# Kernel optimization log

Hardware: AMD Instinct MI355X
Metric: run time of the kernel (lower is better)

## Reference

```python
import jax, jax.numpy as jnp
import numpy as np

B, SEQ_LEN, ENC_IN, C_OUT = 128, 512, 21, 21
PRED_LEN, D_MODEL, N_HEADS, D_FF = 96, 512, 8, 2048
E_LAYERS = 2
PATCH_LEN, STRIDE = 16, 8
NUM_PATCH = (SEQ_LEN - PATCH_LEN) // STRIDE + 1  # 63
MODES = min(32, NUM_PATCH // 2)  # 31 (mode_select='low' -> index = range(MODES))
K_MA = 25
EPS = 1e-5
DH = D_MODEL // N_HEADS  # 64


def setup_inputs() -> dict:
    key = jax.random.key(0)
    ks = jax.random.split(key, 16)
    s = 0.02
    fscale = 1.0 / (D_MODEL * D_MODEL)
    return {
        'x_enc': jax.random.normal(ks[0], (B, SEQ_LEN, ENC_IN), jnp.float32),
        'x_mark_enc': jax.random.normal(ks[1], (B, SEQ_LEN, 4), jnp.float32),
        'x_dec': jax.random.normal(ks[2], (B, 144, ENC_IN), jnp.float32),
        'x_mark_dec': jax.random.normal(ks[3], (B, 144, 4), jnp.float32),
        'patch_W': s * jax.random.normal(ks[4], (D_MODEL, PATCH_LEN * ENC_IN), jnp.float32),
        'patch_b': jnp.zeros((D_MODEL,), jnp.float32),
        'Wq': s * jax.random.normal(ks[5], (E_LAYERS, D_MODEL, D_MODEL), jnp.float32),
        'bq': jnp.zeros((E_LAYERS, D_MODEL), jnp.float32),
        'Wo': s * jax.random.normal(ks[6], (E_LAYERS, D_MODEL, D_MODEL), jnp.float32),
        'bo': jnp.zeros((E_LAYERS, D_MODEL), jnp.float32),
        'four_wr': fscale * jax.random.uniform(ks[7], (E_LAYERS, N_HEADS, DH, DH, MODES), jnp.float32),
        'four_wi': fscale * jax.random.uniform(ks[8], (E_LAYERS, N_HEADS, DH, DH, MODES), jnp.float32),
        'conv1_W': s * jax.random.normal(ks[9], (E_LAYERS, D_FF, D_MODEL), jnp.float32),
        'conv2_W': s * jax.random.normal(ks[10], (E_LAYERS, D_MODEL, D_FF), jnp.float32),
        'norm_gamma': jnp.ones((D_MODEL,), jnp.float32),
        'norm_beta': jnp.zeros((D_MODEL,), jnp.float32),
        'head_W': s * jax.random.normal(ks[11], (PRED_LEN * C_OUT, NUM_PATCH * D_MODEL), jnp.float32),
        'head_b': jnp.zeros((PRED_LEN * C_OUT,), jnp.float32),
        'trend_W': s * jax.random.normal(ks[12], (PRED_LEN, SEQ_LEN), jnp.float32),
        'trend_b': jnp.zeros((PRED_LEN,), jnp.float32),
    }


def series_decomp(x, k=K_MA):
    # x: [B, L, C]; replicate-pad ends by (k-1)//2, moving mean via cumsum
    pad = (k - 1) // 2
    front = jnp.repeat(x[:, :1, :], pad, axis=1)
    end = jnp.repeat(x[:, -1:, :], pad, axis=1)
    xp = jnp.concatenate([front, x, end], axis=1)
    c = jnp.cumsum(xp, axis=1)
    c = jnp.concatenate([jnp.zeros_like(c[:, :1]), c], axis=1)
    mean = (c[:, k:] - c[:, :-k]) / k
    return x - mean, mean


def my_layernorm(x, g, b):
    mu = x.mean(-1, keepdims=True)
    var = ((x - mu) ** 2).mean(-1, keepdims=True)
    xh = (x - mu) / jnp.sqrt(var + EPS) * g + b
    return xh - xh.mean(axis=1, keepdims=True)


def fourier_block(q, wr, wi):
    # q: [B, L, H, E] -> torch FourierBlock (low-freq modes 0..MODES-1)
    Bq, L, H, E = q.shape
    xs = q.transpose(0, 2, 3, 1)                       # [B,H,E,L]
    x_ft = jnp.fft.rfft(xs, axis=-1)                   # [B,H,E,L//2+1]
    W = wr + 1j * wi                                   # [H,E,F,M] complex
    out_sel = jnp.einsum('bhem,hefm->bhfm', x_ft[..., :MODES], W)
    out_ft = jnp.zeros(x_ft.shape, x_ft.dtype).at[..., :MODES].set(out_sel)
    y = jnp.fft.irfft(out_ft, n=L, axis=-1)            # [B,H,E,L]
    # torch does out.view(B, L, -1) on contiguous [B,H,E,L]; flat reshape is identical
    return y.reshape(Bq, L, H * E)


def encoder_layer(x, Wq_l, bq_l, Wo_l, bo_l, wr, wi, c1, c2):
    Bq, L, D = x.shape
    q = (x @ Wq_l.T + bq_l).reshape(Bq, L, N_HEADS, DH)
    new_x = fourier_block(q, wr, wi) @ Wo_l.T + bo_l
    x, _ = series_decomp(x + new_x)
    y = jax.nn.gelu(x @ c1.T, approximate=False) @ c2.T  # conv1d k=1 == matmul, no bias
    res, _ = series_decomp(x + y)
    return res


def _forward(x_enc, patch_W, patch_b, Wq, bq, Wo, bo, four_wr, four_wi,
             conv1_W, conv2_W, norm_gamma, norm_beta, head_W, head_b, trend_W, trend_b):
    seasonal, trend = series_decomp(x_enc)
    # trend_projection over time axis: [B,L,C] -> [B,P,C]
    trend_out = jnp.einsum('blc,pl->bpc', trend, trend_W) + trend_b[None, :, None]
    # patching (unfold over time per channel, then mix channels)
    xs = seasonal.transpose(0, 2, 1)                   # [B,N,L]
    idx = STRIDE * jnp.arange(NUM_PATCH)[:, None] + jnp.arange(PATCH_LEN)[None, :]
    xp = xs[:, :, idx]                                 # [B,N,P,plen]
    xp = xp.transpose(0, 2, 1, 3).reshape(B, NUM_PATCH, ENC_IN * PATCH_LEN)
    enc = xp @ patch_W.T + patch_b                     # [B,P,D]
    for l in range(E_LAYERS):
        enc = encoder_layer(enc, Wq[l], bq[l], Wo[l], bo[l],
                            four_wr[l], four_wi[l], conv1_W[l], conv2_W[l])
    enc = my_layernorm(enc, norm_gamma, norm_beta)
    seasonal_out = (enc.reshape(B, -1) @ head_W.T + head_b).reshape(B, PRED_LEN, C_OUT)
    return seasonal_out + trend_out


def reference(x_enc, x_mark_enc, x_dec, x_mark_dec, patch_W, patch_b, Wq, bq, Wo, bo,
              four_wr, four_wi, conv1_W, conv2_W, norm_gamma, norm_beta,
              head_W, head_b, trend_W, trend_b):
    # x_mark_enc / x_dec / x_mark_dec are accepted but unused, as in the torch forward
    return _forward(x_enc, patch_W, patch_b, Wq, bq, Wo, bo, four_wr, four_wi,
                    conv1_W, conv2_W, norm_gamma, norm_beta, head_W, head_b, trend_W, trend_b)
```

## Files before the change

### kernel.cpp

```cpp
#include <hip/hip_runtime.h>
#include <math.h>

#define B_ 128
#define T_ 512
#define C_ 21
#define L_ 63
#define D_ 512
#define H_ 8
#define DH_ 64
#define MODES_ 31
#define FF_ 2048
#define P_ 96
#define KMA 25
#define PAD 12
#define NOUT (P_*C_)
#define KHEAD (L_*D_)
#define ML (B_*L_)

typedef __attribute__((ext_vector_type(8))) short short8;
typedef __attribute__((ext_vector_type(4))) float f32x4;

__device__ __forceinline__ unsigned short f2b(float f) {
    union { float f; unsigned u; } v; v.f = f;
    unsigned r = v.u + 0x7FFFu + ((v.u >> 16) & 1u);
    return (unsigned short)(r >> 16);
}
__device__ __forceinline__ float b2f(unsigned short u) {
    union { unsigned u; float f; } v; v.u = ((unsigned)u) << 16;
    return v.f;
}
__device__ __forceinline__ void gld_lds16(const void* g, void* l) {
    __builtin_amdgcn_global_load_lds(
        (const __attribute__((address_space(1))) unsigned int*)g,
        (__attribute__((address_space(3))) unsigned int*)l, 16, 0, 0);
}

__global__ void prep_k(const float* __restrict__ Wq, const float* __restrict__ Wo,
                       const float* __restrict__ c1, const float* __restrict__ c2,
                       unsigned short* __restrict__ WqB, unsigned short* __restrict__ WoB,
                       unsigned short* __restrict__ c1B, unsigned short* __restrict__ c2B,
                       const float* __restrict__ pW, unsigned short* __restrict__ pWB,
                       float* __restrict__ cosT, float* __restrict__ sinT) {
    int i = blockIdx.x * 256 + threadIdx.x;
    if (i < 262144) {
        const float* src = (i < 131072) ? Wq : Wo;
        unsigned short* dst = (i < 131072) ? WqB : WoB;
        int j = i & 131071;
        float4 v = ((const float4*)src)[j];
        uint2 p; p.x = (unsigned)f2b(v.x) | ((unsigned)f2b(v.y) << 16);
        p.y = (unsigned)f2b(v.z) | ((unsigned)f2b(v.w) << 16);
        ((uint2*)dst)[j] = p;
    } else if (i < 1310720) {
        int j = i - 262144;
        const float* src = (j < 524288) ? c1 : c2;
        unsigned short* dst = (j < 524288) ? c1B : c2B;
        j &= 524287;
        float4 v = ((const float4*)src)[j];
        uint2 p; p.x = (unsigned)f2b(v.x) | ((unsigned)f2b(v.y) << 16);
        p.y = (unsigned)f2b(v.z) | ((unsigned)f2b(v.w) << 16);
        ((uint2*)dst)[j] = p;
    } else if (i < 1359872) {
        int j = i - 1310720;
        int row = j / 96, c4 = j % 96;
        uint2 p; p.x = 0; p.y = 0;
        if (c4 < 84) {
            float4 v = *(const float4*)(pW + (size_t)row * 336 + c4 * 4);
            p.x = (unsigned)f2b(v.x) | ((unsigned)f2b(v.y) << 16);
            p.y = (unsigned)f2b(v.z) | ((unsigned)f2b(v.w) << 16);
        }
        ((uint2*)pWB)[j] = p;
    } else if (i < 1361888) {
        int j = i - 1359872;
        int m = j / 63, l = j % 63;
        if (m >= MODES_) { cosT[j] = 0.f; sinT[j] = 0.f; }
        else {
            int r = (m * l) % 63;
            double a = 6.283185307179586476925286766559 * (double)r / 63.0;
            cosT[j] = (float)cos(a); sinT[j] = (float)sin(a);
        }
    }
}

__global__ void decomp_input_k(const float* __restrict__ x,
                               unsigned short* __restrict__ seasB,
                               unsigned short* __restrict__ trendB) {
    int idx = blockIdx.x * 256 + threadIdx.x;
    if (idx >= B_ * C_ * 16) return;
    int tc = idx & 15; int rc = idx >> 4; int c = rc % C_; int b = rc / C_;
    const float* xb = x + (size_t)b * T_ * C_ + c;
    int t0 = tc * 32;
    float sum = 0.f;
    #pragma unroll
    for (int i = -PAD; i <= PAD; ++i) {
        int tt = t0 + i; tt = tt < 0 ? 0 : (tt > T_-1 ? T_-1 : tt);
        sum += xb[(size_t)tt * C_];
    }
    for (int t = t0; t < t0 + 32; ++t) {
        float mean = sum * (1.f / KMA);
        float xv = xb[(size_t)t * C_];
        size_t o = ((size_t)b * T_ + t) * C_ + c;
        seasB[o]  = f2b(xv - mean);
        trendB[o] = f2b(mean);
        int add = t + 13 > T_-1 ? T_-1 : t + 13;
        int rem = t - 12 < 0 ? 0 : t - 12;
        sum += xb[(size_t)add * C_] - xb[(size_t)rem * C_];
    }
}

__global__ void patches_k(const unsigned short* __restrict__ seasB,
                          unsigned short* __restrict__ xpB) {
    int idx = blockIdx.x * 256 + threadIdx.x;
    if (idx >= B_*L_*384) return;
    int col = idx % 384; int r = idx / 384; int n = r % L_; int b = r / L_;
    unsigned short v = 0;
    if (col < 336) {
        int c = col >> 4; int j = col & 15;
        v = seasB[((size_t)b * T_ + 8*n + j) * C_ + c];
    }
    xpB[idx] = v;
}

__global__ __launch_bounds__(256) void trend_mfma(
    const unsigned short* __restrict__ trendB, const float* __restrict__ tW,
    const float* __restrict__ tb, const float* __restrict__ hb,
    float* __restrict__ outT)
{
    __shared__ unsigned short Asl[64*32];
    __shared__ unsigned short Wsl[96*32];
    int bm = blockIdx.x;
    int t = threadIdx.x, wave = t >> 6, lane = t & 63;
    int wr = wave >> 1, wc = wave & 1, g2 = lane >> 4, rl = lane & 15;
    f32x4 acc[2][3] = {};
    int ar = t >> 2, aslot = t & 3;
    int rowg = bm*64 + ar; int ab = rowg / 21, ac = rowg % 21;
    for (int k0 = 0; k0 < 512; k0 += 32) {
        __syncthreads();
        {
            unsigned short vals[8];
            int kb = k0 + aslot*8;
            #pragma unroll
            for (int j = 0; j < 8; ++j)
                vals[j] = trendB[((size_t)ab * T_ + kb + j) * C_ + ac];
            int phys = aslot ^ ((ar>>1)&3);
            *(uint4*)&Asl[ar*32 + phys*8] = *(const uint4*)vals;
        }
        #pragma unroll
        for (int i = 0; i < 3; ++i) {
            int idx = t + 256*i;
            int r = idx >> 3, c4 = idx & 7;
            float4 w4 = *(const float4*)(tW + (size_t)r * T_ + k0 + c4*4);
            uint2 p; p.x = (unsigned)f2b(w4.x) | ((unsigned)f2b(w4.y) << 16);
            p.y = (unsigned)f2b(w4.z) | ((unsigned)f2b(w4.w) << 16);
            *(uint2*)&Wsl[r*32 + (((c4>>1) ^ ((r>>1)&3)) << 3) + ((c4&1) << 2)] = p;
        }
        __syncthreads();
        short8 af[2], wf[3];
        #pragma unroll
        for (int m = 0; m < 2; ++m) {
            int r = wr*32 + m*16 + rl;
            af[m] = *(const short8*)&Asl[r*32 + ((g2 ^ ((r>>1)&3)) << 3)];
        }
        #pragma unroll
        for (int n = 0; n < 3; ++n) {
            int r = wc*48 + n*16 + rl;
            wf[n] = *(const short8*)&Wsl[r*32 + ((g2 ^ ((r>>1)&3)) << 3)];
        }
        #pragma unroll
        for (int m = 0; m < 2; ++m)
            #pragma unroll
            for (int n = 0; n < 3; ++n)
                acc[m][n] = __builtin_amdgcn_mfma_f32_16x16x32_bf16(af[m], wf[n], acc[m][n], 0,0,0);
    }
    #pragma unroll
    for (int n = 0; n < 3; ++n) {
        int p = wc*48 + n*16 + rl;
        float bias = tb[p];
        #pragma unroll
        for (int m = 0; m < 2; ++m)
            #pragma unroll
            for (int j = 0; j < 4; ++j) {
                int rg = bm*64 + wr*32 + m*16 + g2*4 + j;
                int b = rg / 21, c = rg % 21;
                outT[(size_t)b * NOUT + p*21 + c] = acc[m][n][j] + bias + hb[p*21 + c];
            }
    }
}

__global__ __launch_bounds__(256) void gemm_mfma(
    const unsigned short* __restrict__ A,
    const unsigned short* __restrict__ W,
    const float* __restrict__ bias,
    float* __restrict__ Cf,
    unsigned short* __restrict__ Cb,
    int M, int N, int K, int act)
{
    __shared__ unsigned short Asl[2][64*64];
    __shared__ unsigned short Wsl[2][128*64];
    int bm = blockIdx.y, bn = blockIdx.x;
    int t = threadIdx.x;
    int wave = t >> 6, lane = t & 63;
    int wr = wave >> 1, wc = wave & 1;
    int g2 = lane >> 4, rl = lane & 15;
    int lr8 = lane >> 3, l7 = lane & 7;
    f32x4 acc[2][4] = {};
    const unsigned short* Ab = A + (size_t)(bm*64) * K;
    const unsigned short* Wb = W + (size_t)(bn*128) * K;

    #pragma unroll
    for (int i = 0; i < 2; ++i) {
        int seg = wave*2 + i;
        int r = seg*8 + lr8;
        int ko = (l7 ^ (r & 7)) << 3;
        gld_lds16(Ab + (size_t)r*K + ko, &Asl[0][seg*512]);
    }
    #pragma unroll
    for (int i = 0; i < 4; ++i) {
        int seg = wave*4 + i;
        int r = seg*8 + lr8;
        int ko = (l7 ^ (r & 7)) << 3;
        gld_lds16(Wb + (size_t)r*K + ko, &Wsl[0][seg*512]);
    }

    int cur = 0;
    for (int k0 = 0; k0 < K; k0 += 64, cur ^= 1) {
        __syncthreads();
        if (k0 + 64 < K) {
            int kn = k0 + 64;
            #pragma unroll
            for (int i = 0; i < 2; ++i) {
                int seg = wave*2 + i;
                int r = seg*8 + lr8;
                int ko = (l7 ^ (r & 7)) << 3;
                gld_lds16(Ab + (size_t)r*K + kn + ko, &Asl[cur^1][seg*512]);
            }
            #pragma unroll
            for (int i = 0; i < 4; ++i) {
                int seg = wave*4 + i;
                int r = seg*8 + lr8;
                int ko = (l7 ^ (r & 7)) << 3;
                gld_lds16(Wb + (size_t)r*K + kn + ko, &Wsl[cur^1][seg*512]);
            }
        }
        short8 af[2][2], wf[2][4];
        #pragma unroll
        for (int sub = 0; sub < 2; ++sub) {
            #pragma unroll
            for (int m = 0; m < 2; ++m) {
                int r = wr*32 + m*16 + rl;
                af[sub][m] = *(const short8*)&Asl[cur][r*64 + (((sub*4+g2) ^ (r&7)) << 3)];
            }
            #pragma unroll
            for (int n = 0; n < 4; ++n) {
                int r = wc*64 + n*16 + rl;
                wf[sub][n] = *(const short8*)&Wsl[cur][r*64 + (((sub*4+g2) ^ (r&7)) << 3)];
            }
        }
        #pragma unroll
        for (int sub = 0; sub < 2; ++sub)
            #pragma unroll
            for (int m = 0; m < 2; ++m)
                #pragma unroll
                for (int n = 0; n < 4; ++n)
                    acc[m][n] = __builtin_amdgcn_mfma_f32_16x16x32_bf16(af[sub][m], wf[sub][n], acc[m][n], 0,0,0);
    }

    int crow0 = bm*64 + wr*32;
    int ccol0 = bn*128 + wc*64;
    #pragma unroll
    for (int n = 0; n < 4; ++n) {
        int col = ccol0 + n*16 + rl;
        float bv = bias ? bias[col] : 0.f;
        #pragma unroll
        for (int m = 0; m < 2; ++m) {
            #pragma unroll
            for (int j = 0; j < 4; ++j) {
                int row = crow0 + m*16 + g2*4 + j;
                float x = acc[m][n][j] + bv;
                if (act == 1) x = 0.5f * x * (1.f + erff(x * 0.70710678118654752f));
                size_t ix = (size_t)row * N + col;
                if (Cf) Cf[ix] = x;
                if (Cb) Cb[ix] = f2b(x);
            }
        }
    }
}

__global__ __launch_bounds__(256) void fourier1_k(
    const float* __restrict__ q, const float* __restrict__ cosT, const float* __restrict__ sinT,
    float* __restrict__ Xre_g, float* __restrict__ Xim_g)
{
    __shared__ float qs[63][64];
    __shared__ float ct[2016], st[2016];
    int b = blockIdx.x >> 3, h = blockIdx.x & 7;
    int t = threadIdx.x;
    for (int idx = t; idx < 1008; idx += 256) {
        int l = idx >> 4, e4 = idx & 15;
        *(float4*)&qs[l][e4*4] = *(const float4*)(q + ((size_t)(b*63 + l))*512 + h*64 + e4*4);
    }
    for (int idx = t; idx < 504; idx += 256) {
        *(float4*)&ct[idx*4] = *(const float4*)(cosT + idx*4);
        *(float4*)&st[idx*4] = *(const float4*)(sinT + idx*4);
    }
    __syncthreads();
    int mm = t & 31, g = t >> 5;
    float re[8] = {}, im[8] = {};
    for (int l = 0; l < 63; ++l) {
        float c = ct[mm*63 + l], s = st[mm*63 + l];
        #pragma unroll
        for (int j = 0; j < 8; ++j) {
            float v = qs[l][g*8 + j];
            re[j] = fmaf(v, c, re[j]);
            im[j] = fmaf(-v, s, im[j]);
        }
    }
    if (mm < MODES_) {
        size_t base = ((size_t)(h*MODES_ + mm)*128 + b)*64 + g*8;
        *(float4*)&Xre_g[base]   = *(float4*)&re[0];
        *(float4*)&Xre_g[base+4] = *(float4*)&re[4];
        *(float4*)&Xim_g[base]   = *(float4*)&im[0];
        *(float4*)&Xim_g[base+4] = *(float4*)&im[4];
    }
}

__global__ __launch_bounds__(256) void fourier2_k(
    const float* __restrict__ Xre_g, const float* __restrict__ Xim_g,
    const float* __restrict__ wr, const float* __restrict__ wi,
    float* __restrict__ Ore_g, float* __restrict__ Oim_g)
{
    __shared__ unsigned short Xr[128*64], Xi[128*64];
    __shared__ unsigned short Wr[64*64], Wi[64*64], Wn[64*64];
    int h = blockIdx.x / MODES_, mm = blockIdx.x % MODES_;
    int t = threadIdx.x;
    size_t xbase = ((size_t)(h*MODES_ + mm)) * 128 * 64;
    #pragma unroll
    for (int i = 0; i < 8; ++i) {
        int idx = t + 256*i;
        int r = idx >> 4, c4 = idx & 15;
        int ad = r*64 + (((c4>>1) ^ (r&7)) << 3) + ((c4&1) << 2);
        float4 v = *(const float4*)(Xre_g + xbase + (size_t)r*64 + c4*4);
        uint2 p; p.x = (unsigned)f2b(v.x) | ((unsigned)f2b(v.y) << 16);
        p.y = (unsigned)f2b(v.z) | ((unsigned)f2b(v.w) << 16);
        *(uint2*)&Xr[ad] = p;
        v = *(const float4*)(Xim_g + xbase + (size_t)r*64 + c4*4);
        p.x = (unsigned)f2b(v.x) | ((unsigned)f2b(v.y) << 16);
        p.y = (unsigned)f2b(v.z) | ((unsigned)f2b(v.w) << 16);
        *(uint2*)&Xi[ad] = p;
    }
    #pragma unroll
    for (int i = 0; i < 2; ++i) {
        int idx = t + 256*i;
        int f = idx >> 3, oct = idx & 7;
        unsigned short wrv[8], wiv[8], wnv[8];
        #pragma unroll
        for (int j = 0; j < 8; ++j) {
            int e = oct*8 + j;
            size_t a = (((size_t)(h*64 + e))*64 + f)*MODES_ + mm;
            wrv[j] = f2b(wr[a]);
            wiv[j] = f2b(wi[a]);
            wnv[j] = wiv[j] ^ 0x8000u;
        }
        int ad = f*64 + ((oct ^ (f&7)) << 3);
        *(uint4*)&Wr[ad] = *(const uint4*)wrv;
        *(uint4*)&Wi[ad] = *(const uint4*)wiv;
        *(uint4*)&Wn[ad] = *(const uint4*)wnv;
    }
    __syncthreads();
    int wave = t >> 6, lane = t & 63;
    int wv = wave >> 1, wc = wave & 1;
    int g2 = lane >> 4, rl = lane & 15;
    f32x4 ar[4][2] = {}, ai[4][2] = {};
    #pragma unroll
    for (int sub = 0; sub < 2; ++sub) {
        short8 xr[4], xi[4], br[2], bi[2], bn[2];
        #pragma unroll
        for (int m = 0; m < 4; ++m) {
            int r = wv*64 + m*16 + rl;
            int off = r*64 + (((sub*4+g2) ^ (r&7)) << 3);
            xr[m] = *(const short8*)&Xr[off];
            xi[m] = *(const short8*)&Xi[off];
        }
        #pragma unroll
        for (int n = 0; n < 2; ++n) {
            int r = wc*32 + n*16 + rl;
            int off = r*64 + (((sub*4+g2) ^ (r&7)) << 3);
            br[n] = *(const short8*)&Wr[off];
            bi[n] = *(const short8*)&Wi[off];
            bn[n] = *(const short8*)&Wn[off];
        }
        #pragma unroll
        for (int m = 0; m < 4; ++m)
            #pragma unroll
            for (int n = 0; n < 2; ++n) {
                ar[m][n] = __builtin_amdgcn_mfma_f32_16x16x32_bf16(xr[m], br[n], ar[m][n], 0,0,0);
                ar[m][n] = __builtin_amdgcn_mfma_f32_16x16x32_bf16(xi[m], bn[n], ar[m][n], 0,0,0);
                ai[m][n] = __builtin_amdgcn_mfma_f32_16x16x32_bf16(xr[m], bi[n], ai[m][n], 0,0,0);
                ai[m][n] = __builtin_amdgcn_mfma_f32_16x16x32_bf16(xi[m], br[n], ai[m][n], 0,0,0);
            }
    }
    #pragma unroll
    for (int m = 0; m < 4; ++m)
        #pragma unroll
        for (int n = 0; n < 2; ++n)
            #pragma unroll
            for (int j = 0; j < 4; ++j) {
                int b = wv*64 + m*16 + g2*4 + j;
                int f = wc*32 + n*16 + rl;
                Ore_g[xbase + (size_t)b*64 + f] = ar[m][n][j];
                Oim_g[xbase + (size_t)b*64 + f] = ai[m][n][j];
            }
}

__global__ __launch_bounds__(256) void fourier3_k(
    const float* __restrict__ Ore_g, const float* __restrict__ Oim_g,
    const float* __restrict__ cosT, const float* __restrict__ sinT,
    unsigned short* __restrict__ yB)
{
    __shared__ float Ore[31][64], Oim[31][64];
    __shared__ float ct[2016], st[2016];
    int b = blockIdx.x >> 3, h = blockIdx.x & 7;
    int t = threadIdx.x;
    for (int idx = t; idx < 496; idx += 256) {
        int m = idx >> 4, e4 = idx & 15;
        size_t a = ((size_t)(h*MODES_ + m)*128 + b)*64 + e4*4;
        *(float4*)&Ore[m][e4*4] = *(const float4*)(Ore_g + a);
        *(float4*)&Oim[m][e4*4] = *(const float4*)(Oim_g + a);
    }
    for (int idx = t; idx < 504; idx += 256) {
        *(float4*)&ct[idx*4] = *(const float4*)(cosT + idx*4);
        *(float4*)&st[idx*4] = *(const float4*)(sinT + idx*4);
    }
    __syncthreads();
    int f = t & 63, w = t >> 6;
    int l0 = w*16;
    float y[16];
    float r0 = Ore[0][f];
    #pragma unroll
    for (int i = 0; i < 16; ++i) y[i] = r0;
    for (int m = 1; m < MODES_; ++m) {
        float re2 = 2.f*Ore[m][f], im2 = 2.f*Oim[m][f];
        #pragma unroll
        for (int i = 0; i < 16; ++i) {
            y[i] = fmaf(re2, ct[m*63 + l0 + i], y[i]);
            y[i] = fmaf(-im2, st[m*63 + l0 + i], y[i]);
        }
    }
    int nl = (w == 3) ? 15 : 16;
    unsigned short* yo = yB + ((size_t)(b*512) + h*64 + f) * 63 + l0;
    for (int i = 0; i < nl; ++i) yo[i] = f2b(y[i] * (1.f/63.f));
}

__global__ void decomp_add_k(const unsigned short* __restrict__ X,
                             const unsigned short* __restrict__ Yv,
                             unsigned short* __restrict__ outB) {
    int idx = blockIdx.x * 256 + threadIdx.x;
    if (idx >= B_*D_) return;
    int b = idx >> 9, d = idx & 511;
    const unsigned short* xp = X  + (size_t)b * L_ * D_ + d;
    const unsigned short* yp = Yv + (size_t)b * L_ * D_ + d;
    unsigned short* ob = outB + (size_t)b * L_ * D_ + d;
    #define RD(l) (b2f(xp[(size_t)(l) * D_]) + b2f(yp[(size_t)(l) * D_]))
    float sum = 13.f * RD(0);
    #pragma unroll
    for (int j = 1; j <= 12; ++j) sum += RD(j);
    for (int l = 0; l < L_; ++l) {
        float res = RD(l) - sum * (1.f / KMA);
        ob[(size_t)l * D_] = f2b(res);
        int add = l + 13 > L_-1 ? L_-1 : l + 13;
        int rem = l - 12 < 0 ? 0 : l - 12;
        sum += RD(add) - RD(rem);
    }
    #undef RD
}

__global__ __launch_bounds__(256) void ln_colmean_k(
    const unsigned short* __restrict__ Xb, const float* __restrict__ g,
    const float* __restrict__ bt, unsigned short* __restrict__ outB)
{
    __shared__ unsigned short lds[63][512];
    int b = blockIdx.x;
    int w = threadIdx.x >> 6, lane = threadIdx.x & 63;
    for (int i = 0; i < 16; ++i) {
        int row = w*16 + i;
        if (row >= 63) break;
        const unsigned short* x = Xb + ((size_t)(b*63 + row))*512 + lane*8;
        uint4 raw = *(const uint4*)x;
        const unsigned short* rp = (const unsigned short*)&raw;
        float v[8]; float s = 0.f, s2 = 0.f;
        #pragma unroll
        for (int j = 0; j < 8; ++j) { v[j] = b2f(rp[j]); s += v[j]; s2 += v[j]*v[j]; }
        #pragma unroll
        for (int o = 32; o > 0; o >>= 1) { s += __shfl_down(s, o); s2 += __shfl_down(s2, o); }
        s = __shfl(s, 0); s2 = __shfl(s2, 0);
        float mu = s * (1.f/D_);
        float var = s2 * (1.f/D_) - mu*mu;
        float rs = rsqrtf(var + 1e-5f);
        unsigned short o16[8];
        #pragma unroll
        for (int j = 0; j < 8; ++j) {
            int d = lane*8 + j;
            o16[j] = f2b((v[j] - mu) * rs * g[d] + bt[d]);
        }
        *(uint4*)&lds[row][lane*8] = *(const uint4*)o16;
    }
    __syncthreads();
    #pragma unroll
    for (int i = 0; i < 2; ++i) {
        int d = threadIdx.x + 256*i;
        float s = 0.f;
        for (int l = 0; l < 63; ++l) s += b2f(lds[l][d]);
        s *= (1.f / 63.f);
        for (int l = 0; l < 63; ++l)
            outB[((size_t)(b*63 + l))*512 + d] = f2b(b2f(lds[l][d]) - s);
    }
}

__global__ __launch_bounds__(256) void head_mfma(
    const unsigned short* __restrict__ A,
    const float* __restrict__ W,
    float* __restrict__ parts)
{
    __shared__ float red[128][48];
    int nt = blockIdx.x;
    int kc = blockIdx.y;
    int wv = threadIdx.x >> 6, lane = threadIdx.x & 63;
    int rl = lane & 15, g2 = lane >> 4;
    f32x4 acc[8][3] = {};
    const unsigned short* Ab = A + (size_t)rl * KHEAD;
    const float* Wb = W + (size_t)(nt*48 + rl) * KHEAD;
    int kbeg = kc*2688 + wv*672 + g2*8;

    for (int ks = 0; ks < 21; ++ks) {
        int k = kbeg + ks*32;
        short8 af[8];
        #pragma unroll
        for (int m = 0; m < 8; ++m)
            af[m] = *(const short8*)(Ab + (size_t)(m*16) * KHEAD + k);
        short8 wf[3];
        #pragma unroll
        for (int n = 0; n < 3; ++n) {
            float4 lo = *(const float4*)(Wb + (size_t)(n*16) * KHEAD + k);
            float4 hi = *(const float4*)(Wb + (size_t)(n*16) * KHEAD + k + 4);
            unsigned short u[8] = { f2b(lo.x), f2b(lo.y), f2b(lo.z), f2b(lo.w),
                                    f2b(hi.x), f2b(hi.y), f2b(hi.z), f2b(hi.w) };
            wf[n] = *(const short8*)u;
        }
        #pragma unroll
        for (int m = 0; m < 8; ++m)
            #pragma unroll
            for (int n = 0; n < 3; ++n)
                acc[m][n] = __builtin_amdgcn_mfma_f32_16x16x32_bf16(af[m], wf[n], acc[m][n], 0,0,0);
    }

    for (int w = 0; w < 4; ++w) {
        if (wv == w) {
            #pragma unroll
            for (int m = 0; m < 8; ++m)
                #pragma unroll
                for (int n = 0; n < 3; ++n)
                    #pragma unroll
                    for (int j = 0; j < 4; ++j) {
                        int row = m*16 + g2*4 + j, col = n*16 + rl;
                        if (w == 0) red[row][col] = acc[m][n][j];
                        else        red[row][col] += acc[m][n][j];
                    }
        }
        __syncthreads();
    }
    float* pout = parts + (size_t)kc * (B_*NOUT);
    for (int idx = threadIdx.x; idx < 128*48; idx += 256) {
        int row = idx / 48, col = idx % 48;
        pout[(size_t)row * NOUT + nt*48 + col] = red[row][col];
    }
}

__global__ void reduce_k(const float* __restrict__ trendout, const float* __restrict__ parts,
                         float* __restrict__ out) {
    int i = blockIdx.x * 256 + threadIdx.x;
    if (i >= 64512) return;
    float4 s = ((const float4*)trendout)[i];
    for (int kc = 0; kc < 12; ++kc) {
        float4 p = ((const float4*)parts)[(size_t)kc * 64512 + i];
        s.x += p.x; s.y += p.y; s.z += p.z; s.w += p.w;
    }
    ((float4*)out)[i] = s;
}

extern "C" void kernel_launch(void* const* d_in, const int* in_sizes, int n_in,
                              void* d_out, int out_size, void* d_ws, size_t ws_size,
                              hipStream_t stream) {
    const float* x_enc   = (const float*)d_in[0];
    const float* patch_W = (const float*)d_in[4];
    const float* patch_b = (const float*)d_in[5];
    const float* Wq      = (const float*)d_in[6];
    const float* bq      = (const float*)d_in[7];
    const float* Wo      = (const float*)d_in[8];
    const float* bo      = (const float*)d_in[9];
    const float* four_wr = (const float*)d_in[10];
    const float* four_wi = (const float*)d_in[11];
    const float* c1      = (const float*)d_in[12];
    const float* c2      = (const float*)d_in[13];
    const float* gamma   = (const float*)d_in[14];
    const float* beta    = (const float*)d_in[15];
    const float* head_W  = (const float*)d_in[16];
    const float* head_b  = (const float*)d_in[17];
    const float* trend_W = (const float*)d_in[18];
    const float* trend_b = (const float*)d_in[19];
    float* out = (float*)d_out;
    float* ws  = (float*)d_ws;

    unsigned short* seasB  = (unsigned short*)ws;
    unsigned short* trendB = (unsigned short*)(ws + 688128);
    unsigned short* xpB    = (unsigned short*)(ws + 1376256);
    unsigned short* bufAb  = (unsigned short*)(ws + 2924544);
    unsigned short* tmpB16 = (unsigned short*)(ws + 4988928);
    unsigned short* tmp2   = (unsigned short*)(ws + 7053312);
    unsigned short* bufCb  = (unsigned short*)(ws + 9117696);
    float* qF    = ws + 11182080;
    float* Ore_g = qF;
    float* Oim_g = qF + 2031616;
    float* big   = ws + 15310848;
    unsigned short* hidB = (unsigned short*)big;
    float* Xre_g = big;
    float* Xim_g = big + 2031616;
    unsigned short* WqB = (unsigned short*)(ws + 23568384);
    unsigned short* WoB = (unsigned short*)(ws + 23830528);
    unsigned short* c1B = (unsigned short*)(ws + 24092672);
    unsigned short* c2B = (unsigned short*)(ws + 25141248);
    unsigned short* pWB = (unsigned short*)(ws + 26189824);
    float* cosT = ws + 26288128;
    float* sinT = ws + 26290144;
    float* trendout = ws + 26292160;
    float* parts = ws + 26550208;

    auto cdiv = [](int a, int b) { return (a + b - 1) / b; };

    prep_k<<<5321,256,0,stream>>>(Wq, Wo, c1, c2, WqB, WoB, c1B, c2B, patch_W, pWB, cosT, sinT);
    decomp_input_k<<<cdiv(B_*C_*16,256),256,0,stream>>>(x_enc, seasB, trendB);
    patches_k<<<cdiv(B_*L_*384,256),256,0,stream>>>(seasB, xpB);
    trend_mfma<<<42,256,0,stream>>>(trendB, trend_W, trend_b, head_b, trendout);

    gemm_mfma<<<dim3(4,126),256,0,stream>>>(xpB, pWB, patch_b, (float*)nullptr, bufAb, ML, 512, 384, 0);

    for (int l = 0; l < 2; ++l) {
        const unsigned short* WqB_l = WqB + (size_t)l*512*512;
        const unsigned short* WoB_l = WoB + (size_t)l*512*512;
        const unsigned short* c1B_l = c1B + (size_t)l*FF_*D_;
        const unsigned short* c2B_l = c2B + (size_t)l*D_*FF_;
        const float* bq_l = bq + (size_t)l*512;
        const float* bo_l = bo + (size_t)l*512;
        const float* wr_l = four_wr + (size_t)l*H_*DH_*DH_*MODES_;
        const float* wi_l = four_wi + (size_t)l*H_*DH_*DH_*MODES_;

        gemm_mfma<<<dim3(4,126),256,0,stream>>>(bufAb, WqB_l, bq_l, qF, (unsigned short*)nullptr, ML, 512, 512, 0);
        fourier1_k<<<B_*H_,256,0,stream>>>(qF, cosT, sinT, Xre_g, Xim_g);
        fourier2_k<<<H_*MODES_,256,0,stream>>>(Xre_g, Xim_g, wr_l, wi_l, Ore_g, Oim_g);
        fourier3_k<<<B_*H_,256,0,stream>>>(Ore_g, Oim_g, cosT, sinT, tmpB16);
        gemm_mfma<<<dim3(4,126),256,0,stream>>>(tmpB16, WoB_l, bo_l, (float*)nullptr, tmp2, ML, 512, 512, 0);
        decomp_add_k<<<cdiv(B_*D_,256),256,0,stream>>>(bufAb, tmp2, bufCb);
        gemm_mfma<<<dim3(16,126),256,0,stream>>>(bufCb, c1B_l, (const float*)nullptr, (float*)nullptr, hidB, ML, FF_, 512, 1);
        gemm_mfma<<<dim3(4,126),256,0,stream>>>(hidB, c2B_l, (const float*)nullptr, (float*)nullptr, tmp2, ML, 512, FF_, 0);
        decomp_add_k<<<cdiv(B_*D_,256),256,0,stream>>>(bufCb, tmp2, bufAb);
    }

    ln_colmean_k<<<B_,256,0,stream>>>(bufAb, gamma, beta, tmpB16);
    head_mfma<<<dim3(42,12),256,0,stream>>>(tmpB16, head_W, parts);
    reduce_k<<<cdiv(64512,256),256,0,stream>>>(trendout, parts, out);
}
```

Measured before the change: 556.1 us.

## Split-K Wo/conv2 GEMMs and trend GEMM, fuse decomp with patch extraction

Adds a split-K dimension to the generic GEMM, used with two K-chunks for the Wo and conv2 projections. The two bf16 partial outputs are summed inside decomp_add_k, which now also holds the 63-row column in registers instead of re-reading it. The trend GEMM is split four ways and writes into the head partials buffer, so one reduce covers both. Input decomposition and patch extraction are fused into one per-batch kernel through LDS. The aim is more blocks in flight for the GEMMs that had only 504 blocks, and fewer launches and round trips through memory. The cost is extra partial-sum traffic and bf16 rounding of partial sums before they are added.

```diff
diff --git a/kernel.cpp b/kernel.cpp
--- a/kernel.cpp
+++ b/kernel.cpp
@@ -81,59 +81,57 @@
     }
 }
 
-__global__ void decomp_input_k(const float* __restrict__ x,
-                               unsigned short* __restrict__ seasB,
-                               unsigned short* __restrict__ trendB) {
-    int idx = blockIdx.x * 256 + threadIdx.x;
-    if (idx >= B_ * C_ * 16) return;
-    int tc = idx & 15; int rc = idx >> 4; int c = rc % C_; int b = rc / C_;
-    const float* xb = x + (size_t)b * T_ * C_ + c;
-    int t0 = tc * 32;
-    float sum = 0.f;
-    #pragma unroll
-    for (int i = -PAD; i <= PAD; ++i) {
-        int tt = t0 + i; tt = tt < 0 ? 0 : (tt > T_-1 ? T_-1 : tt);
-        sum += xb[(size_t)tt * C_];
-    }
-    for (int t = t0; t < t0 + 32; ++t) {
-        float mean = sum * (1.f / KMA);
-        float xv = xb[(size_t)t * C_];
-        size_t o = ((size_t)b * T_ + t) * C_ + c;
-        seasB[o]  = f2b(xv - mean);
-        trendB[o] = f2b(mean);
-        int add = t + 13 > T_-1 ? T_-1 : t + 13;
-        int rem = t - 12 < 0 ? 0 : t - 12;
-        sum += xb[(size_t)add * C_] - xb[(size_t)rem * C_];
-    }
-}
-
-__global__ void patches_k(const unsigned short* __restrict__ seasB,
-                          unsigned short* __restrict__ xpB) {
-    int idx = blockIdx.x * 256 + threadIdx.x;
-    if (idx >= B_*L_*384) return;
-    int col = idx % 384; int r = idx / 384; int n = r % L_; int b = r / L_;
-    unsigned short v = 0;
-    if (col < 336) {
-        int c = col >> 4; int j = col & 15;
-        v = seasB[((size_t)b * T_ + 8*n + j) * C_ + c];
-    }
-    xpB[idx] = v;
+__global__ __launch_bounds__(256) void decomp_patches_k(
+    const float* __restrict__ x,
+    unsigned short* __restrict__ trendB,
+    unsigned short* __restrict__ xpB)
+{
+    __shared__ unsigned short seas[21][512];
+    int b = blockIdx.x;
+    const float* xb0 = x + (size_t)b * T_ * C_;
+    for (int task = threadIdx.x; task < 336; task += 256) {
+        int c = task / 16, tc = task % 16;
+        const float* xb = xb0 + c;
+        int t0 = tc * 32;
+        float sum = 0.f;
+        #pragma unroll
+        for (int i = -PAD; i <= PAD; ++i) {
+            int tt = t0 + i; tt = tt < 0 ? 0 : (tt > T_-1 ? T_-1 : tt);
+            sum += xb[(size_t)tt * C_];
+        }
+        for (int t = t0; t < t0 + 32; ++t) {
+            float mean = sum * (1.f / KMA);
+            float xv = xb[(size_t)t * C_];
+            seas[c][t] = f2b(xv - mean);
+            trendB[((size_t)b * T_ + t) * C_ + c] = f2b(mean);
+            int add = t + 13 > T_-1 ? T_-1 : t + 13;
+            int rem = t - 12 < 0 ? 0 : t - 12;
+            sum += xb[(size_t)add * C_] - xb[(size_t)rem * C_];
+        }
+    }
+    __syncthreads();
+    for (int idx = threadIdx.x; idx < 63*384; idx += 256) {
+        int n = idx / 384, col = idx % 384;
+        unsigned short v = 0;
+        if (col < 336) { int c = col >> 4, j = col & 15; v = seas[c][8*n + j]; }
+        xpB[((size_t)b * 63 + n) * 384 + col] = v;
+    }
 }
 
 __global__ __launch_bounds__(256) void trend_mfma(
     const unsigned short* __restrict__ trendB, const float* __restrict__ tW,
     const float* __restrict__ tb, const float* __restrict__ hb,
-    float* __restrict__ outT)
+    float* __restrict__ parts)
 {
     __shared__ unsigned short Asl[64*32];
     __shared__ unsigned short Wsl[96*32];
-    int bm = blockIdx.x;
+    int bm = blockIdx.x, kc = blockIdx.y;
     int t = threadIdx.x, wave = t >> 6, lane = t & 63;
     int wr = wave >> 1, wc = wave & 1, g2 = lane >> 4, rl = lane & 15;
     f32x4 acc[2][3] = {};
     int ar = t >> 2, aslot = t & 3;
     int rowg = bm*64 + ar; int ab = rowg / 21, ac = rowg % 21;
-    for (int k0 = 0; k0 < 512; k0 += 32) {
+    for (int k0 = kc*128; k0 < kc*128 + 128; k0 += 32) {
         __syncthreads();
         {
             unsigned short vals[8];
@@ -171,17 +169,19 @@
             for (int n = 0; n < 3; ++n)
                 acc[m][n] = __builtin_amdgcn_mfma_f32_16x16x32_bf16(af[m], wf[n], acc[m][n], 0,0,0);
     }
+    float* outT = parts + (size_t)kc * (B_*NOUT);
     #pragma unroll
     for (int n = 0; n < 3; ++n) {
         int p = wc*48 + n*16 + rl;
-        float bias = tb[p];
         #pragma unroll
         for (int m = 0; m < 2; ++m)
             #pragma unroll
             for (int j = 0; j < 4; ++j) {
                 int rg = bm*64 + wr*32 + m*16 + g2*4 + j;
                 int b = rg / 21, c = rg % 21;
-                outT[(size_t)b * NOUT + p*21 + c] = acc[m][n][j] + bias + hb[p*21 + c];
+                float v = acc[m][n][j];
+                if (kc == 0) v += tb[p] + hb[p*21 + c];
+                outT[(size_t)b * NOUT + p*21 + c] = v;
             }
     }
 }
@@ -192,33 +192,33 @@
     const float* __restrict__ bias,
     float* __restrict__ Cf,
     unsigned short* __restrict__ Cb,
-    int M, int N, int K, int act)
+    int M, int N, int K, int lda, int ldw, int act)
 {
     __shared__ unsigned short Asl[2][64*64];
     __shared__ unsigned short Wsl[2][128*64];
-    int bm = blockIdx.y, bn = blockIdx.x;
+    int bm = blockIdx.y, bn = blockIdx.x, kc = blockIdx.z;
     int t = threadIdx.x;
     int wave = t >> 6, lane = t & 63;
     int wr = wave >> 1, wc = wave & 1;
     int g2 = lane >> 4, rl = lane & 15;
     int lr8 = lane >> 3, l7 = lane & 7;
     f32x4 acc[2][4] = {};
-    const unsigned short* Ab = A + (size_t)(bm*64) * K;
-    const unsigned short* Wb = W + (size_t)(bn*128) * K;
+    const unsigned short* Ab = A + (size_t)(bm*64) * lda + (size_t)kc * K;
+    const unsigned short* Wb = W + (size_t)(bn*128) * ldw + (size_t)kc * K;
 
     #pragma unroll
     for (int i = 0; i < 2; ++i) {
         int seg = wave*2 + i;
         int r = seg*8 + lr8;
         int ko = (l7 ^ (r & 7)) << 3;
-        gld_lds16(Ab + (size_t)r*K + ko, &Asl[0][seg*512]);
+        gld_lds16(Ab + (size_t)r*lda + ko, &Asl[0][seg*512]);
     }
     #pragma unroll
     for (int i = 0; i < 4; ++i) {
         int seg = wave*4 + i;
         int r = seg*8 + lr8;
         int ko = (l7 ^ (r & 7)) << 3;
-        gld_lds16(Wb + (size_t)r*K + ko, &Wsl[0][seg*512]);
+        gld_lds16(Wb + (size_t)r*ldw + ko, &Wsl[0][seg*512]);
     }
 
     int cur = 0;
@@ -231,14 +231,14 @@
                 int seg = wave*2 + i;
                 int r = seg*8 + lr8;
                 int ko = (l7 ^ (r & 7)) << 3;
-                gld_lds16(Ab + (size_t)r*K + kn + ko, &Asl[cur^1][seg*512]);
+                gld_lds16(Ab + (size_t)r*lda + kn + ko, &Asl[cur^1][seg*512]);
             }
             #pragma unroll
             for (int i = 0; i < 4; ++i) {
                 int seg = wave*4 + i;
                 int r = seg*8 + lr8;
                 int ko = (l7 ^ (r & 7)) << 3;
-                gld_lds16(Wb + (size_t)r*K + kn + ko, &Wsl[cur^1][seg*512]);
+                gld_lds16(Wb + (size_t)r*ldw + kn + ko, &Wsl[cur^1][seg*512]);
             }
         }
         short8 af[2][2], wf[2][4];
@@ -266,10 +266,11 @@
 
     int crow0 = bm*64 + wr*32;
     int ccol0 = bn*128 + wc*64;
+    size_t obase = (size_t)kc * M * N;
     #pragma unroll
     for (int n = 0; n < 4; ++n) {
         int col = ccol0 + n*16 + rl;
-        float bv = bias ? bias[col] : 0.f;
+        float bv = (bias && kc == 0) ? bias[col] : 0.f;
         #pragma unroll
         for (int m = 0; m < 2; ++m) {
             #pragma unroll
@@ -277,7 +278,7 @@
                 int row = crow0 + m*16 + g2*4 + j;
                 float x = acc[m][n][j] + bv;
                 if (act == 1) x = 0.5f * x * (1.f + erff(x * 0.70710678118654752f));
-                size_t ix = (size_t)row * N + col;
+                size_t ix = obase + (size_t)row * N + col;
                 if (Cf) Cf[ix] = x;
                 if (Cb) Cb[ix] = f2b(x);
             }
@@ -450,26 +451,30 @@
 }
 
 __global__ void decomp_add_k(const unsigned short* __restrict__ X,
-                             const unsigned short* __restrict__ Yv,
+                             const unsigned short* __restrict__ Y1,
+                             const unsigned short* __restrict__ Y2,
                              unsigned short* __restrict__ outB) {
     int idx = blockIdx.x * 256 + threadIdx.x;
     if (idx >= B_*D_) return;
     int b = idx >> 9, d = idx & 511;
     const unsigned short* xp = X  + (size_t)b * L_ * D_ + d;
-    const unsigned short* yp = Yv + (size_t)b * L_ * D_ + d;
+    const unsigned short* y1 = Y1 + (size_t)b * L_ * D_ + d;
+    const unsigned short* y2 = Y2 + (size_t)b * L_ * D_ + d;
     unsigned short* ob = outB + (size_t)b * L_ * D_ + d;
-    #define RD(l) (b2f(xp[(size_t)(l) * D_]) + b2f(yp[(size_t)(l) * D_]))
-    float sum = 13.f * RD(0);
-    #pragma unroll
-    for (int j = 1; j <= 12; ++j) sum += RD(j);
-    for (int l = 0; l < L_; ++l) {
-        float res = RD(l) - sum * (1.f / KMA);
-        ob[(size_t)l * D_] = f2b(res);
-        int add = l + 13 > L_-1 ? L_-1 : l + 13;
+    float v[63];
+    #pragma unroll
+    for (int l = 0; l < 63; ++l)
+        v[l] = b2f(xp[(size_t)l*D_]) + b2f(y1[(size_t)l*D_]) + b2f(y2[(size_t)l*D_]);
+    float sum = 13.f * v[0];
+    #pragma unroll
+    for (int j = 1; j <= 12; ++j) sum += v[j];
+    #pragma unroll
+    for (int l = 0; l < 63; ++l) {
+        ob[(size_t)l*D_] = f2b(v[l] - sum * (1.f / KMA));
+        int add = l + 13 > 62 ? 62 : l + 13;
         int rem = l - 12 < 0 ? 0 : l - 12;
-        sum += RD(add) - RD(rem);
-    }
-    #undef RD
+        sum += v[add] - v[rem];
+    }
 }
 
 __global__ __launch_bounds__(256) void ln_colmean_k(
@@ -566,19 +571,18 @@
         }
         __syncthreads();
     }
-    float* pout = parts + (size_t)kc * (B_*NOUT);
+    float* pout = parts + (size_t)(4 + kc) * (B_*NOUT);
     for (int idx = threadIdx.x; idx < 128*48; idx += 256) {
         int row = idx / 48, col = idx % 48;
         pout[(size_t)row * NOUT + nt*48 + col] = red[row][col];
     }
 }
 
-__global__ void reduce_k(const float* __restrict__ trendout, const float* __restrict__ parts,
-                         float* __restrict__ out) {
+__global__ void reduce_k(const float* __restrict__ parts, float* __restrict__ out) {
     int i = blockIdx.x * 256 + threadIdx.x;
     if (i >= 64512) return;
-    float4 s = ((const float4*)trendout)[i];
-    for (int kc = 0; kc < 12; ++kc) {
+    float4 s = {0.f, 0.f, 0.f, 0.f};
+    for (int kc = 0; kc < 16; ++kc) {
         float4 p = ((const float4*)parts)[(size_t)kc * 64512 + i];
         s.x += p.x; s.y += p.y; s.z += p.z; s.w += p.w;
     }
@@ -608,38 +612,36 @@
     float* out = (float*)d_out;
     float* ws  = (float*)d_ws;
 
-    unsigned short* seasB  = (unsigned short*)ws;
-    unsigned short* trendB = (unsigned short*)(ws + 688128);
-    unsigned short* xpB    = (unsigned short*)(ws + 1376256);
-    unsigned short* bufAb  = (unsigned short*)(ws + 2924544);
-    unsigned short* tmpB16 = (unsigned short*)(ws + 4988928);
-    unsigned short* tmp2   = (unsigned short*)(ws + 7053312);
-    unsigned short* bufCb  = (unsigned short*)(ws + 9117696);
-    float* qF    = ws + 11182080;
+    unsigned short* trendB = (unsigned short*)ws;
+    unsigned short* xpB    = (unsigned short*)(ws + 700000);
+    unsigned short* bufAb  = (unsigned short*)(ws + 2300000);
+    unsigned short* tmpB16 = (unsigned short*)(ws + 4400000);
+    unsigned short* tmp2   = (unsigned short*)(ws + 6500000);
+    unsigned short* bufCb  = (unsigned short*)(ws + 10700000);
+    float* qF    = ws + 12800000;
     float* Ore_g = qF;
     float* Oim_g = qF + 2031616;
-    float* big   = ws + 15310848;
+    float* big   = ws + 17000000;
     unsigned short* hidB = (unsigned short*)big;
     float* Xre_g = big;
     float* Xim_g = big + 2031616;
-    unsigned short* WqB = (unsigned short*)(ws + 23568384);
-    unsigned short* WoB = (unsigned short*)(ws + 23830528);
-    unsigned short* c1B = (unsigned short*)(ws + 24092672);
-    unsigned short* c2B = (unsigned short*)(ws + 25141248);
-    unsigned short* pWB = (unsigned short*)(ws + 26189824);
-    float* cosT = ws + 26288128;
-    float* sinT = ws + 26290144;
-    float* trendout = ws + 26292160;
-    float* parts = ws + 26550208;
+    unsigned short* WqB = (unsigned short*)(ws + 25300000);
+    unsigned short* WoB = (unsigned short*)(ws + 25600000);
+    unsigned short* c1B = (unsigned short*)(ws + 25900000);
+    unsigned short* c2B = (unsigned short*)(ws + 27000000);
+    unsigned short* pWB = (unsigned short*)(ws + 28100000);
+    float* cosT  = ws + 28200000;
+    float* sinT  = ws + 28210000;
+    float* parts = ws + 28250000;
 
     auto cdiv = [](int a, int b) { return (a + b - 1) / b; };
 
     prep_k<<<5321,256,0,stream>>>(Wq, Wo, c1, c2, WqB, WoB, c1B, c2B, patch_W, pWB, cosT, sinT);
-    decomp_input_k<<<cdiv(B_*C_*16,256),256,0,stream>>>(x_enc, seasB, trendB);
-    patches_k<<<cdiv(B_*L_*384,256),256,0,stream>>>(seasB, xpB);
-    trend_mfma<<<42,256,0,stream>>>(trendB, trend_W, trend_b, head_b, trendout);
-
-    gemm_mfma<<<dim3(4,126),256,0,stream>>>(xpB, pWB, patch_b, (float*)nullptr, bufAb, ML, 512, 384, 0);
+    decomp_patches_k<<<B_,256,0,stream>>>(x_enc, trendB, xpB);
+    trend_mfma<<<dim3(42,4),256,0,stream>>>(trendB, trend_W, trend_b, head_b, parts);
+
+    gemm_mfma<<<dim3(4,126,1),256,0,stream>>>(xpB, pWB, patch_b, (float*)nullptr, bufAb,
+                                              ML, 512, 384, 384, 384, 0);
 
     for (int l = 0; l < 2; ++l) {
         const unsigned short* WqB_l = WqB + (size_t)l*512*512;
@@ -651,18 +653,22 @@
         const float* wr_l = four_wr + (size_t)l*H_*DH_*DH_*MODES_;
         const float* wi_l = four_wi + (size_t)l*H_*DH_*DH_*MODES_;
 
-        gemm_mfma<<<dim3(4,126),256,0,stream>>>(bufAb, WqB_l, bq_l, qF, (unsigned short*)nullptr, ML, 512, 512, 0);
+        gemm_mfma<<<dim3(4,126,1),256,0,stream>>>(bufAb, WqB_l, bq_l, qF, (unsigned short*)nullptr,
+                                                  ML, 512, 512, 512, 512, 0);
         fourier1_k<<<B_*H_,256,0,stream>>>(qF, cosT, sinT, Xre_g, Xim_g);
         fourier2_k<<<H_*MODES_,256,0,stream>>>(Xre_g, Xim_g, wr_l, wi_l, Ore_g, Oim_g);
         fourier3_k<<<B_*H_,256,0,stream>>>(Ore_g, Oim_g, cosT, sinT, tmpB16);
-        gemm_mfma<<<dim3(4,126),256,0,stream>>>(tmpB16, WoB_l, bo_l, (float*)nullptr, tmp2, ML, 512, 512, 0);
-        decomp_add_k<<<cdiv(B_*D_,256),256,0,stream>>>(bufAb, tmp2, bufCb);
-        gemm_mfma<<<dim3(16,126),256,0,stream>>>(bufCb, c1B_l, (const float*)nullptr, (float*)nullptr, hidB, ML, FF_, 512, 1);
-        gemm_mfma<<<dim3(4,126),256,0,stream>>>(hidB, c2B_l, (const float*)nullptr, (float*)nullptr, tmp2, ML, 512, FF_, 0);
-        decomp_add_k<<<cdiv(B_*D_,256),256,0,stream>>>(bufCb, tmp2, bufAb);
+        gemm_mfma<<<dim3(4,126,2),256,0,stream>>>(tmpB16, WoB_l, bo_l, (float*)nullptr, tmp2,
+                                                  ML, 512, 256, 512, 512, 0);
+        decomp_add_k<<<cdiv(B_*D_,256),256,0,stream>>>(bufAb, tmp2, tmp2 + (size_t)ML*512, bufCb);
+        gemm_mfma<<<dim3(16,126,1),256,0,stream>>>(bufCb, c1B_l, (const float*)nullptr, (float*)nullptr, hidB,
+                                                   ML, FF_, 512, 512, 512, 1);
+        gemm_mfma<<<dim3(4,126,2),256,0,stream>>>(hidB, c2B_l, (const float*)nullptr, (float*)nullptr, tmp2,
+                                                  ML, 512, 1024, 2048, 2048, 0);
+        decomp_add_k<<<cdiv(B_*D_,256),256,0,stream>>>(bufCb, tmp2, tmp2 + (size_t)ML*512, bufAb);
     }
 
     ln_colmean_k<<<B_,256,0,stream>>>(bufAb, gamma, beta, tmpB16);
     head_mfma<<<dim3(42,12),256,0,stream>>>(tmpB16, head_W, parts);
-    reduce_k<<<cdiv(64512,256),256,0,stream>>>(trendout, parts, out);
-}
+    reduce_k<<<cdiv(64512,256),256,0,stream>>>(parts, out);
+}
```

Measured after the change: 546.1 us, median of 2. Within noise of the previous version (-1.8%).
